# Optimization experiments

Hardware: AMD Instinct MI355X
Metric: run time of the kernel (lower is better)

Reference implementation:

```python
import math
import jax, jax.numpy as jnp
import numpy as np

D, DK, DV = 256, 256, 256

def setup_inputs() -> dict:
    key = jax.random.key(0)
    ks = jax.random.split(key, 7)
    s = 1.0 / math.sqrt(D)
    return {
        "x": jax.random.normal(ks[0], (4, 4096, D), dtype=jnp.float32),
        "Wq": jax.random.uniform(ks[1], (D, DK), jnp.float32, -s, s),
        "bq": jax.random.uniform(ks[2], (DK,), jnp.float32, -s, s),
        "Wk": jax.random.uniform(ks[3], (D, DK), jnp.float32, -s, s),
        "bk": jax.random.uniform(ks[4], (DK,), jnp.float32, -s, s),
        "Wv": jax.random.uniform(ks[5], (D, DV), jnp.float32, -s, s),
        "bv": jax.random.uniform(ks[6], (DV,), jnp.float32, -s, s),
    }

def reference(x, Wq, bq, Wk, bk, Wv, bv):
    # x: [B, S, D]
    q = x @ Wq + bq            # [B, S, DK]
    k = x @ Wk + bk            # [B, S, DK]
    v = x @ Wv + bv            # [B, S, DV]
    scores = jnp.einsum('bqd,bkd->bqk', q, k) / math.sqrt(DK)  # [B, S, S]
    S = x.shape[1]
    causal = jnp.tril(jnp.ones((S, S), dtype=bool))  # True = keep
    scores = jnp.where(causal, scores, -jnp.inf)
    attn = jax.nn.softmax(scores, axis=-1)
    return jnp.einsum('bqk,bkd->bqd', attn, v)  # [B, S, DV]
```

## Files before the change

### kernel.cpp

```cpp
#include <hip/hip_runtime.h>
#include <cmath>

#define LOG2E 1.4426950408889634f

typedef __attribute__((ext_vector_type(8))) __bf16 bf16x8;
typedef __attribute__((ext_vector_type(4))) float f32x4;
typedef __attribute__((ext_vector_type(16))) float f32x16;
typedef __attribute__((ext_vector_type(4))) float float4v;
typedef __attribute__((ext_vector_type(8))) unsigned short ushort8;
typedef __attribute__((ext_vector_type(4))) unsigned int uint4v;
typedef __attribute__((ext_vector_type(2))) int int2v;

__device__ __forceinline__ unsigned short f2bf(float f) {
  unsigned int u = __builtin_bit_cast(unsigned int, f);
  u += 0x7fffu + ((u >> 16) & 1u);
  return (unsigned short)(u >> 16);
}

__device__ __forceinline__ unsigned int cvtpk(float lo, float hi) {
  unsigned int r;
  asm volatile("v_cvt_pk_bf16_f32 %0, %1, %2" : "=v"(r) : "v"(lo), "v"(hi));
  return r;
}

__device__ __forceinline__ void gload_lds16(const unsigned short* g, unsigned short* l) {
  __builtin_amdgcn_global_load_lds(
      (const __attribute__((address_space(1))) unsigned int*)(const void*)g,
      (__attribute__((address_space(3))) unsigned int*)(void*)l, 16, 0, 0);
}

__global__ __launch_bounds__(256) void prep_w_kernel(
    const float* __restrict__ Wq, const float* __restrict__ Wk,
    const float* __restrict__ Wv, unsigned short* __restrict__ Wt) {
  const int w = blockIdx.y, n = blockIdx.x, k = threadIdx.x;
  const float* W = (w == 0) ? Wq : ((w == 1) ? Wk : Wv);
  const float s = (w == 0) ? (LOG2E / 16.0f) : 1.0f;
  Wt[w * 65536 + n * 256 + k] = f2bf(W[k * 256 + n] * s);
}

__global__ __launch_bounds__(256) void proj_kernel(
    const float* __restrict__ x, const unsigned short* __restrict__ Wt,
    const float* __restrict__ bq, const float* __restrict__ bk,
    const float* __restrict__ bv,
    unsigned short* __restrict__ q_o, unsigned short* __restrict__ k_o,
    unsigned short* __restrict__ vt_o) {
  const int mt = blockIdx.x;
  const int tid = threadIdx.x;
  const int wid = tid >> 6, lane = tid & 63, g = (lane >> 4) & 3, c = lane & 15;
  const int row_base = mt * 64 + wid * 16;

  bf16x8 a[8];
  const float* xr = x + (size_t)(row_base + c) * 256;
#pragma unroll
  for (int s = 0; s < 8; ++s) {
    const float4v v0 = *(const float4v*)(xr + s * 32 + g * 8);
    const float4v v1 = *(const float4v*)(xr + s * 32 + g * 8 + 4);
    union { bf16x8 v; unsigned short u[8]; } t;
#pragma unroll
    for (int j = 0; j < 4; ++j) { t.u[j] = f2bf(v0[j]); t.u[4 + j] = f2bf(v1[j]); }
    a[s] = t.v;
  }

  const unsigned short* w0 = Wt;
  const unsigned short* w1 = Wt + 65536;
  const unsigned short* w2 = Wt + 131072;

#pragma unroll
  for (int nf = 0; nf < 16; ++nf) {
    f32x4 aq = (f32x4){0.f, 0.f, 0.f, 0.f};
    f32x4 ak = (f32x4){0.f, 0.f, 0.f, 0.f};
    f32x4 av = (f32x4){0.f, 0.f, 0.f, 0.f};
    const unsigned short* r0 = w0 + (size_t)(nf * 16 + c) * 256;
    const unsigned short* r1 = w1 + (size_t)(nf * 16 + c) * 256;
    const unsigned short* r2 = w2 + (size_t)(nf * 16 + c) * 256;
#pragma unroll
    for (int s = 0; s < 8; ++s) {
      bf16x8 b0 = *(const bf16x8*)(r0 + s * 32 + g * 8);
      bf16x8 b1 = *(const bf16x8*)(r1 + s * 32 + g * 8);
      bf16x8 b2 = *(const bf16x8*)(r2 + s * 32 + g * 8);
      aq = __builtin_amdgcn_mfma_f32_16x16x32_bf16(a[s], b0, aq, 0, 0, 0);
      ak = __builtin_amdgcn_mfma_f32_16x16x32_bf16(a[s], b1, ak, 0, 0, 0);
      av = __builtin_amdgcn_mfma_f32_16x16x32_bf16(a[s], b2, av, 0, 0, 0);
    }
    const float bql = bq[nf * 16 + c] * (LOG2E / 16.0f);
    const float bkl = bk[nf * 16 + c];
    const float bvl = bv[nf * 16 + c];
#pragma unroll
    for (int r = 0; r < 4; ++r) {
      const int row = row_base + g * 4 + r;
      q_o[(size_t)row * 256 + nf * 16 + c] = f2bf(aq[r] + bql);
      k_o[(size_t)row * 256 + nf * 16 + c] = f2bf(ak[r] + bkl);
      const int b_ = row >> 12, s_ = row & 4095;
      vt_o[((size_t)b_ * 256 + nf * 16 + c) * 4096 + s_] = f2bf(av[r] + bvl);
    }
  }
}

__global__ __launch_bounds__(256, 2) void attn_kernel(
    const unsigned short* __restrict__ qg, const unsigned short* __restrict__ kg,
    const unsigned short* __restrict__ vtg, float* __restrict__ out) {
  __shared__ unsigned short Klds[64 * 256];
  __shared__ unsigned short Vlds[256 * 64];
  __shared__ float llds[2][32];

  const int tid = threadIdx.x;
  const int wid = tid >> 6, lane = tid & 63;
  const int hi = lane >> 5, q5 = lane & 31;
  const int wk = wid & 1, dh = wid >> 1;
  const int bid = blockIdx.x;
  const int half = bid >> 8, k6 = (bid >> 2) & 63, b = bid & 3;
  const int qt = half ? k6 : 127 - k6;
  const int T = (qt >> 1) + 1;

  const unsigned short* qb = qg + (size_t)b * 4096 * 256;
  const unsigned short* kb = kg + (size_t)b * 4096 * 256;
  const unsigned short* vb = vtg + (size_t)b * 256 * 4096;
  float* outb = out + (size_t)b * 4096 * 256;

  const int q0 = qt * 32;
  const int qrow = q0 + q5;

  int koff[8], voff[8];
#pragma unroll
  for (int i = 0; i < 8; ++i) {
    const int kr = wid * 16 + i * 2 + (lane >> 5);
    const int c8 = (lane & 31) ^ (kr & 7);
    koff[i] = kr * 256 + c8 * 8;
    const int d = wid * 64 + i * 8 + (lane >> 3);
    const int c8v = (lane & 7) ^ (d & 7);
    voff[i] = d * 4096 + c8v * 8;
  }

  auto stage = [&](int t) {
    const unsigned short* kp = kb + t * (64 * 256);
    const unsigned short* vp = vb + t * 64;
#pragma unroll
    for (int i = 0; i < 8; ++i)
      gload_lds16(kp + koff[i], &Klds[(wid * 8 + i) * 512]);
#pragma unroll
    for (int i = 0; i < 8; ++i)
      gload_lds16(vp + voff[i], &Vlds[(wid * 8 + i) * 512]);
  };

  bf16x8 bqf[16];
  {
    const unsigned short* qr = qb + (size_t)qrow * 256;
#pragma unroll
    for (int s = 0; s < 16; ++s) bqf[s] = *(const bf16x8*)(qr + s * 16 + hi * 8);
  }

  float l = 0.f;
  f32x16 o[4];
#pragma unroll
  for (int d = 0; d < 4; ++d)
#pragma unroll
    for (int r = 0; r < 16; ++r) o[d][r] = 0.f;

  const int krow = wk * 32 + q5;
  const int ksw = (krow & 7) << 3;
  const int kbase = krow * 256;

  int kcolr[16];
#pragma unroll
  for (int r = 0; r < 16; ++r) kcolr[r] = wk * 32 + (r & 3) + 8 * (r >> 2) + 4 * hi;

  stage(0);
  for (int t = 0; t < T; ++t) {
    __syncthreads();

    f32x16 sa, sb;
#pragma unroll
    for (int r = 0; r < 16; ++r) { sa[r] = 0.f; sb[r] = 0.f; }
#pragma unroll
    for (int s = 0; s < 8; ++s) {
      bf16x8 ka0 = *(const bf16x8*)(&Klds[(kbase + s * 16 + hi * 8) ^ ksw]);
      bf16x8 ka1 = *(const bf16x8*)(&Klds[(kbase + (s + 8) * 16 + hi * 8) ^ ksw]);
      sa = __builtin_amdgcn_mfma_f32_32x32x16_bf16(ka0, bqf[s], sa, 0, 0, 0);
      sb = __builtin_amdgcn_mfma_f32_32x32x16_bf16(ka1, bqf[s + 8], sb, 0, 0, 0);
    }
    f32x16 sc = sa + sb;

    if (t == T - 1) {
#pragma unroll
      for (int r = 0; r < 16; ++r)
        if (t * 64 + kcolr[r] > qrow) sc[r] = -1e30f;
    }

    float p[16];
#pragma unroll
    for (int r = 0; r < 16; ++r) p[r] = __builtin_amdgcn_exp2f(sc[r]);
    {
      float s0 = (p[0] + p[1]) + (p[2] + p[3]);
      float s1 = (p[4] + p[5]) + (p[6] + p[7]);
      float s2 = (p[8] + p[9]) + (p[10] + p[11]);
      float s3 = (p[12] + p[13]) + (p[14] + p[15]);
      l += (s0 + s1) + (s2 + s3);
    }

    bf16x8 pfrag[2];
#pragma unroll
    for (int s2 = 0; s2 < 2; ++s2) {
      const int base = s2 * 8;
      unsigned int X = cvtpk(p[base + 0], p[base + 1]);
      unsigned int Y = cvtpk(p[base + 2], p[base + 3]);
      unsigned int Z = cvtpk(p[base + 4], p[base + 5]);
      unsigned int W = cvtpk(p[base + 6], p[base + 7]);
#if __has_builtin(__builtin_amdgcn_permlane32_swap)
      int2v rx = __builtin_amdgcn_permlane32_swap((int)X, (int)Z, false, false);
      int2v ry = __builtin_amdgcn_permlane32_swap((int)Y, (int)W, false, false);
      uint4v u = (uint4v){(unsigned)rx[0], (unsigned)ry[0], (unsigned)rx[1], (unsigned)ry[1]};
#else
      const unsigned int Xp = __shfl_xor((int)X, 32);
      const unsigned int Yp = __shfl_xor((int)Y, 32);
      const unsigned int Zp = __shfl_xor((int)Z, 32);
      const unsigned int Wp = __shfl_xor((int)W, 32);
      uint4v u = (uint4v){hi ? Zp : X, hi ? Wp : Y, hi ? Z : Xp, hi ? W : Yp};
#endif
      pfrag[s2] = __builtin_bit_cast(bf16x8, u);
    }

#pragma unroll
    for (int dblk = 0; dblk < 4; ++dblk) {
      const int drow = (dh * 4 + dblk) * 32 + q5;
      const int vsw = (drow & 7) << 3;
      const int vbase = drow * 64 + wk * 32;
#pragma unroll
      for (int s2 = 0; s2 < 2; ++s2) {
        bf16x8 va = *(const bf16x8*)(&Vlds[(vbase + s2 * 16 + hi * 8) ^ vsw]);
        o[dblk] = __builtin_amdgcn_mfma_f32_32x32x16_bf16(va, pfrag[s2], o[dblk], 0, 0, 0);
      }
    }

    if (t + 1 < T) {
      __syncthreads();
      stage(t + 1);
    }
  }

  l += __shfl_xor(l, 32);
  if (dh == 0 && hi == 0) llds[wk][q5] = l;
  __syncthreads();
  const float L = llds[0][q5] + llds[1][q5];
  const float scale = 1.0f / L;

  float* oz = (float*)Klds;
  if (wk == 1) {
#pragma unroll
    for (int dblk = 0; dblk < 4; ++dblk)
#pragma unroll
      for (int r = 0; r < 16; ++r) {
        const int dg = (dh * 4 + dblk) * 32 + (r & 3) + 8 * (r >> 2) + 4 * hi;
        oz[dg * 32 + q5] = o[dblk][r];
      }
  }
  __syncthreads();
  if (wk == 0) {
#pragma unroll
    for (int dblk = 0; dblk < 4; ++dblk) {
#pragma unroll
      for (int q2 = 0; q2 < 4; ++q2) {
        float4v val;
#pragma unroll
        for (int e = 0; e < 4; ++e) {
          const int r = q2 * 4 + e;
          const int dg = (dh * 4 + dblk) * 32 + e + 8 * q2 + 4 * hi;
          val[e] = (o[dblk][r] + oz[dg * 32 + q5]) * scale;
        }
        *(float4v*)(outb + (size_t)qrow * 256 + (dh * 4 + dblk) * 32 + 8 * q2 + 4 * hi) = val;
      }
    }
  }
}

extern "C" void kernel_launch(void* const* d_in, const int* in_sizes, int n_in,
                              void* d_out, int out_size, void* d_ws, size_t ws_size,
                              hipStream_t stream) {
  (void)in_sizes; (void)n_in; (void)out_size; (void)ws_size;
  const float* x  = (const float*)d_in[0];
  const float* Wq = (const float*)d_in[1];
  const float* bq = (const float*)d_in[2];
  const float* Wk = (const float*)d_in[3];
  const float* bk = (const float*)d_in[4];
  const float* Wv = (const float*)d_in[5];
  const float* bv = (const float*)d_in[6];
  float* out = (float*)d_out;

  unsigned short* qs  = (unsigned short*)d_ws;
  unsigned short* ks  = qs  + (size_t)16384 * 256;
  unsigned short* vts = ks  + (size_t)16384 * 256;
  unsigned short* Wt  = vts + (size_t)16384 * 256;

  prep_w_kernel<<<dim3(256, 3), 256, 0, stream>>>(Wq, Wk, Wv, Wt);
  proj_kernel<<<256, 256, 0, stream>>>(x, Wt, bq, bk, bv, qs, ks, vts);
  attn_kernel<<<512, 256, 0, stream>>>(qs, ks, vts, out);
}
```

Measured before the change: 173.1 us.

## Register-prefetch next K/V tile during compute and split projection grid

The attention kernel stops using direct global-to-LDS loads issued after compute. Instead it loads the next K/V tile into registers at the start of each iteration, overlapping the fetch with the QK and PV MFMAs, then writes the tile to swizzled LDS after a barrier. It also raises wave priority around the MFMA blocks and splits the projection kernel over two column halves to double its block count. The cost is extra VGPRs for staging, which may reduce occupancy, and the projection now reconverts x to bf16 twice.

```diff
diff --git a/kernel.cpp b/kernel.cpp
--- a/kernel.cpp
+++ b/kernel.cpp
@@ -23,12 +23,6 @@
   return r;
 }
 
-__device__ __forceinline__ void gload_lds16(const unsigned short* g, unsigned short* l) {
-  __builtin_amdgcn_global_load_lds(
-      (const __attribute__((address_space(1))) unsigned int*)(const void*)g,
-      (__attribute__((address_space(3))) unsigned int*)(void*)l, 16, 0, 0);
-}
-
 __global__ __launch_bounds__(256) void prep_w_kernel(
     const float* __restrict__ Wq, const float* __restrict__ Wk,
     const float* __restrict__ Wv, unsigned short* __restrict__ Wt) {
@@ -45,6 +39,7 @@
     unsigned short* __restrict__ q_o, unsigned short* __restrict__ k_o,
     unsigned short* __restrict__ vt_o) {
   const int mt = blockIdx.x;
+  const int nfh = blockIdx.y;
   const int tid = threadIdx.x;
   const int wid = tid >> 6, lane = tid & 63, g = (lane >> 4) & 3, c = lane & 15;
   const int row_base = mt * 64 + wid * 16;
@@ -66,7 +61,8 @@
   const unsigned short* w2 = Wt + 131072;
 
 #pragma unroll
-  for (int nf = 0; nf < 16; ++nf) {
+  for (int nfi = 0; nfi < 8; ++nfi) {
+    const int nf = nfh * 8 + nfi;
     f32x4 aq = (f32x4){0.f, 0.f, 0.f, 0.f};
     f32x4 ak = (f32x4){0.f, 0.f, 0.f, 0.f};
     f32x4 av = (f32x4){0.f, 0.f, 0.f, 0.f};
@@ -120,26 +116,28 @@
   const int q0 = qt * 32;
   const int qrow = q0 + q5;
 
-  int koff[8], voff[8];
-#pragma unroll
-  for (int i = 0; i < 8; ++i) {
-    const int kr = wid * 16 + i * 2 + (lane >> 5);
-    const int c8 = (lane & 31) ^ (kr & 7);
-    koff[i] = kr * 256 + c8 * 8;
-    const int d = wid * 64 + i * 8 + (lane >> 3);
-    const int c8v = (lane & 7) ^ (d & 7);
-    voff[i] = d * 4096 + c8v * 8;
-  }
-
-  auto stage = [&](int t) {
-    const unsigned short* kp = kb + t * (64 * 256);
-    const unsigned short* vp = vb + t * 64;
-#pragma unroll
-    for (int i = 0; i < 8; ++i)
-      gload_lds16(kp + koff[i], &Klds[(wid * 8 + i) * 512]);
-#pragma unroll
-    for (int i = 0; i < 8; ++i)
-      gload_lds16(vp + voff[i], &Vlds[(wid * 8 + i) * 512]);
+  uint4v kst[8], vst[8];
+  const int krp = lane >> 5, kc8 = lane & 31;
+  const int vrp = lane >> 3, vc8 = lane & 7;
+
+  auto load_tiles = [&](int t) {
+#pragma unroll
+    for (int i = 0; i < 8; ++i) {
+      const int kr = (wid * 8 + i) * 2 + krp;
+      kst[i] = *(const uint4v*)(kb + (size_t)t * 16384 + kr * 256 + kc8 * 8);
+      const int d = (wid * 8 + i) * 8 + vrp;
+      vst[i] = *(const uint4v*)(vb + (size_t)d * 4096 + t * 64 + vc8 * 8);
+    }
+    __builtin_amdgcn_sched_barrier(0);
+  };
+  auto write_tiles = [&]() {
+#pragma unroll
+    for (int i = 0; i < 8; ++i) {
+      const int kr = (wid * 8 + i) * 2 + krp;
+      *(uint4v*)(&Klds[kr * 256 + (kc8 ^ (kr & 7)) * 8]) = kst[i];
+      const int d = (wid * 8 + i) * 8 + vrp;
+      *(uint4v*)(&Vlds[d * 64 + (vc8 ^ (d & 7)) * 8]) = vst[i];
+    }
   };
 
   bf16x8 bqf[16];
@@ -164,13 +162,18 @@
 #pragma unroll
   for (int r = 0; r < 16; ++r) kcolr[r] = wk * 32 + (r & 3) + 8 * (r >> 2) + 4 * hi;
 
-  stage(0);
+  load_tiles(0);
+  write_tiles();
+  __syncthreads();
+
   for (int t = 0; t < T; ++t) {
-    __syncthreads();
+    const bool pf = (t + 1 < T);
+    if (pf) load_tiles(t + 1);
 
     f32x16 sa, sb;
 #pragma unroll
     for (int r = 0; r < 16; ++r) { sa[r] = 0.f; sb[r] = 0.f; }
+    __builtin_amdgcn_s_setprio(1);
 #pragma unroll
     for (int s = 0; s < 8; ++s) {
       bf16x8 ka0 = *(const bf16x8*)(&Klds[(kbase + s * 16 + hi * 8) ^ ksw]);
@@ -178,6 +181,7 @@
       sa = __builtin_amdgcn_mfma_f32_32x32x16_bf16(ka0, bqf[s], sa, 0, 0, 0);
       sb = __builtin_amdgcn_mfma_f32_32x32x16_bf16(ka1, bqf[s + 8], sb, 0, 0, 0);
     }
+    __builtin_amdgcn_s_setprio(0);
     f32x16 sc = sa + sb;
 
     if (t == T - 1) {
@@ -219,6 +223,7 @@
       pfrag[s2] = __builtin_bit_cast(bf16x8, u);
     }
 
+    __builtin_amdgcn_s_setprio(1);
 #pragma unroll
     for (int dblk = 0; dblk < 4; ++dblk) {
       const int drow = (dh * 4 + dblk) * 32 + q5;
@@ -230,10 +235,12 @@
         o[dblk] = __builtin_amdgcn_mfma_f32_32x32x16_bf16(va, pfrag[s2], o[dblk], 0, 0, 0);
       }
     }
-
-    if (t + 1 < T) {
+    __builtin_amdgcn_s_setprio(0);
+
+    __syncthreads();
+    if (pf) {
+      write_tiles();
       __syncthreads();
-      stage(t + 1);
     }
   }
 
@@ -291,6 +298,6 @@
   unsigned short* Wt  = vts + (size_t)16384 * 256;
 
   prep_w_kernel<<<dim3(256, 3), 256, 0, stream>>>(Wq, Wk, Wv, Wt);
-  proj_kernel<<<256, 256, 0, stream>>>(x, Wt, bq, bk, bv, qs, ks, vts);
+  proj_kernel<<<dim3(256, 2), 256, 0, stream>>>(x, Wt, bq, bk, bv, qs, ks, vts);
   attn_kernel<<<512, 256, 0, stream>>>(qs, ks, vts, out);
 }
```

New measurement: 239.3 us. 38.2% more time.

## Double-buffer 32-key attention tiles, drop cross-wave reduction, split projection grid

Applied to the files above, without the earlier changes.

The attention kernel now streams 32-key K/V tiles into two LDS buffers and issues the next tile's load right after the barrier, so loading overlaps compute and one barrier per iteration goes away. Each wave owns 64 output dims over all keys, which removes the final LDS reduction of partial outputs and row sums across waves. The projection kernel is split over two grid columns of output features to double its block count. Smaller key tiles mean more iterations and more loop overhead per query tile, and the V swizzle layout changes.

```diff
diff --git a/kernel.cpp b/kernel.cpp
--- a/kernel.cpp
+++ b/kernel.cpp
@@ -7,7 +7,6 @@
 typedef __attribute__((ext_vector_type(4))) float f32x4;
 typedef __attribute__((ext_vector_type(16))) float f32x16;
 typedef __attribute__((ext_vector_type(4))) float float4v;
-typedef __attribute__((ext_vector_type(8))) unsigned short ushort8;
 typedef __attribute__((ext_vector_type(4))) unsigned int uint4v;
 typedef __attribute__((ext_vector_type(2))) int int2v;
 
@@ -45,6 +44,7 @@
     unsigned short* __restrict__ q_o, unsigned short* __restrict__ k_o,
     unsigned short* __restrict__ vt_o) {
   const int mt = blockIdx.x;
+  const int nfh = blockIdx.y;
   const int tid = threadIdx.x;
   const int wid = tid >> 6, lane = tid & 63, g = (lane >> 4) & 3, c = lane & 15;
   const int row_base = mt * 64 + wid * 16;
@@ -66,7 +66,8 @@
   const unsigned short* w2 = Wt + 131072;
 
 #pragma unroll
-  for (int nf = 0; nf < 16; ++nf) {
+  for (int nfi = 0; nfi < 8; ++nfi) {
+    const int nf = nfh * 8 + nfi;
     f32x4 aq = (f32x4){0.f, 0.f, 0.f, 0.f};
     f32x4 ak = (f32x4){0.f, 0.f, 0.f, 0.f};
     f32x4 av = (f32x4){0.f, 0.f, 0.f, 0.f};
@@ -99,47 +100,46 @@
 __global__ __launch_bounds__(256, 2) void attn_kernel(
     const unsigned short* __restrict__ qg, const unsigned short* __restrict__ kg,
     const unsigned short* __restrict__ vtg, float* __restrict__ out) {
-  __shared__ unsigned short Klds[64 * 256];
-  __shared__ unsigned short Vlds[256 * 64];
-  __shared__ float llds[2][32];
+  __shared__ unsigned short Klds[2][32 * 256];
+  __shared__ unsigned short Vlds[2][256 * 32];
 
   const int tid = threadIdx.x;
   const int wid = tid >> 6, lane = tid & 63;
   const int hi = lane >> 5, q5 = lane & 31;
-  const int wk = wid & 1, dh = wid >> 1;
+  const int dh = wid;
   const int bid = blockIdx.x;
-  const int half = bid >> 8, k6 = (bid >> 2) & 63, b = bid & 3;
-  const int qt = half ? k6 : 127 - k6;
-  const int T = (qt >> 1) + 1;
+  const int c = bid & 255, half = bid >> 8;
+  const int qt = half ? (c >> 2) : (127 - (c >> 2));
+  const int b = c & 3;
+  const int T = qt + 1;
 
   const unsigned short* qb = qg + (size_t)b * 4096 * 256;
   const unsigned short* kb = kg + (size_t)b * 4096 * 256;
   const unsigned short* vb = vtg + (size_t)b * 256 * 4096;
   float* outb = out + (size_t)b * 4096 * 256;
 
-  const int q0 = qt * 32;
-  const int qrow = q0 + q5;
-
-  int koff[8], voff[8];
-#pragma unroll
-  for (int i = 0; i < 8; ++i) {
-    const int kr = wid * 16 + i * 2 + (lane >> 5);
-    const int c8 = (lane & 31) ^ (kr & 7);
-    koff[i] = kr * 256 + c8 * 8;
-    const int d = wid * 64 + i * 8 + (lane >> 3);
-    const int c8v = (lane & 7) ^ (d & 7);
-    voff[i] = d * 4096 + c8v * 8;
-  }
-
-  auto stage = [&](int t) {
-    const unsigned short* kp = kb + t * (64 * 256);
-    const unsigned short* vp = vb + t * 64;
-#pragma unroll
-    for (int i = 0; i < 8; ++i)
-      gload_lds16(kp + koff[i], &Klds[(wid * 8 + i) * 512]);
-#pragma unroll
-    for (int i = 0; i < 8; ++i)
-      gload_lds16(vp + voff[i], &Vlds[(wid * 8 + i) * 512]);
+  const int qrow = qt * 32 + q5;
+
+  int koff[4], voff[4];
+#pragma unroll
+  for (int i = 0; i < 4; ++i) {
+    const int kr = wid * 8 + i * 2 + (lane >> 5);
+    const int cs = (lane & 31) ^ (kr & 7);
+    koff[i] = kr * 256 + cs * 8;
+    const int d = wid * 64 + i * 16 + (lane >> 2);
+    const int cv = (lane & 3) ^ ((d >> 1) & 3);
+    voff[i] = d * 4096 + cv * 8;
+  }
+
+  auto stage = [&](int bufn, int t) {
+    const unsigned short* kp = kb + (size_t)t * 8192;
+    const unsigned short* vp = vb + t * 32;
+#pragma unroll
+    for (int i = 0; i < 4; ++i)
+      gload_lds16(kp + koff[i], &Klds[bufn][(wid * 4 + i) * 512]);
+#pragma unroll
+    for (int i = 0; i < 4; ++i)
+      gload_lds16(vp + voff[i], &Vlds[bufn][(wid * 4 + i) * 512]);
   };
 
   bf16x8 bqf[16];
@@ -150,31 +150,32 @@
   }
 
   float l = 0.f;
-  f32x16 o[4];
-#pragma unroll
-  for (int d = 0; d < 4; ++d)
+  f32x16 o[2];
+#pragma unroll
+  for (int d = 0; d < 2; ++d)
 #pragma unroll
     for (int r = 0; r < 16; ++r) o[d][r] = 0.f;
 
-  const int krow = wk * 32 + q5;
-  const int ksw = (krow & 7) << 3;
-  const int kbase = krow * 256;
+  const int ksw = (q5 & 7) << 3;
+  const int kbase = q5 * 256;
 
   int kcolr[16];
 #pragma unroll
-  for (int r = 0; r < 16; ++r) kcolr[r] = wk * 32 + (r & 3) + 8 * (r >> 2) + 4 * hi;
-
-  stage(0);
+  for (int r = 0; r < 16; ++r) kcolr[r] = (r & 3) + 8 * (r >> 2) + 4 * hi;
+
+  stage(0, 0);
   for (int t = 0; t < T; ++t) {
+    const int bufn = t & 1;
     __syncthreads();
+    if (t + 1 < T) stage(bufn ^ 1, t + 1);
 
     f32x16 sa, sb;
 #pragma unroll
     for (int r = 0; r < 16; ++r) { sa[r] = 0.f; sb[r] = 0.f; }
 #pragma unroll
     for (int s = 0; s < 8; ++s) {
-      bf16x8 ka0 = *(const bf16x8*)(&Klds[(kbase + s * 16 + hi * 8) ^ ksw]);
-      bf16x8 ka1 = *(const bf16x8*)(&Klds[(kbase + (s + 8) * 16 + hi * 8) ^ ksw]);
+      bf16x8 ka0 = *(const bf16x8*)(&Klds[bufn][(kbase + s * 16 + hi * 8) ^ ksw]);
+      bf16x8 ka1 = *(const bf16x8*)(&Klds[bufn][(kbase + (s + 8) * 16 + hi * 8) ^ ksw]);
       sa = __builtin_amdgcn_mfma_f32_32x32x16_bf16(ka0, bqf[s], sa, 0, 0, 0);
       sb = __builtin_amdgcn_mfma_f32_32x32x16_bf16(ka1, bqf[s + 8], sb, 0, 0, 0);
     }
@@ -183,7 +184,7 @@
     if (t == T - 1) {
 #pragma unroll
       for (int r = 0; r < 16; ++r)
-        if (t * 64 + kcolr[r] > qrow) sc[r] = -1e30f;
+        if (t * 32 + kcolr[r] > qrow) sc[r] = -1e30f;
     }
 
     float p[16];
@@ -220,54 +221,29 @@
     }
 
 #pragma unroll
-    for (int dblk = 0; dblk < 4; ++dblk) {
-      const int drow = (dh * 4 + dblk) * 32 + q5;
-      const int vsw = (drow & 7) << 3;
-      const int vbase = drow * 64 + wk * 32;
+    for (int dblk = 0; dblk < 2; ++dblk) {
+      const int drow = dh * 64 + dblk * 32 + q5;
+      const int vsw = (drow >> 1) & 3;
 #pragma unroll
       for (int s2 = 0; s2 < 2; ++s2) {
-        bf16x8 va = *(const bf16x8*)(&Vlds[(vbase + s2 * 16 + hi * 8) ^ vsw]);
+        const int chunk = s2 * 2 + hi;
+        bf16x8 va = *(const bf16x8*)(&Vlds[bufn][drow * 32 + ((chunk ^ vsw) * 8)]);
         o[dblk] = __builtin_amdgcn_mfma_f32_32x32x16_bf16(va, pfrag[s2], o[dblk], 0, 0, 0);
       }
     }
-
-    if (t + 1 < T) {
-      __syncthreads();
-      stage(t + 1);
-    }
   }
 
   l += __shfl_xor(l, 32);
-  if (dh == 0 && hi == 0) llds[wk][q5] = l;
-  __syncthreads();
-  const float L = llds[0][q5] + llds[1][q5];
-  const float scale = 1.0f / L;
-
-  float* oz = (float*)Klds;
-  if (wk == 1) {
-#pragma unroll
-    for (int dblk = 0; dblk < 4; ++dblk)
-#pragma unroll
-      for (int r = 0; r < 16; ++r) {
-        const int dg = (dh * 4 + dblk) * 32 + (r & 3) + 8 * (r >> 2) + 4 * hi;
-        oz[dg * 32 + q5] = o[dblk][r];
-      }
-  }
-  __syncthreads();
-  if (wk == 0) {
-#pragma unroll
-    for (int dblk = 0; dblk < 4; ++dblk) {
-#pragma unroll
-      for (int q2 = 0; q2 < 4; ++q2) {
-        float4v val;
-#pragma unroll
-        for (int e = 0; e < 4; ++e) {
-          const int r = q2 * 4 + e;
-          const int dg = (dh * 4 + dblk) * 32 + e + 8 * q2 + 4 * hi;
-          val[e] = (o[dblk][r] + oz[dg * 32 + q5]) * scale;
-        }
-        *(float4v*)(outb + (size_t)qrow * 256 + (dh * 4 + dblk) * 32 + 8 * q2 + 4 * hi) = val;
-      }
+  const float scale = 1.0f / l;
+#pragma unroll
+  for (int dblk = 0; dblk < 2; ++dblk) {
+#pragma unroll
+    for (int q2 = 0; q2 < 4; ++q2) {
+      float4v val;
+#pragma unroll
+      for (int e = 0; e < 4; ++e) val[e] = o[dblk][q2 * 4 + e] * scale;
+      const int d0 = dh * 64 + dblk * 32 + 8 * q2 + 4 * hi;
+      *(float4v*)(outb + (size_t)qrow * 256 + d0) = val;
     }
   }
 }
@@ -291,6 +267,6 @@
   unsigned short* Wt  = vts + (size_t)16384 * 256;
 
   prep_w_kernel<<<dim3(256, 3), 256, 0, stream>>>(Wq, Wk, Wv, Wt);
-  proj_kernel<<<256, 256, 0, stream>>>(x, Wt, bq, bk, bv, qs, ks, vts);
+  proj_kernel<<<dim3(256, 2), 256, 0, stream>>>(x, Wt, bq, bk, bv, qs, ks, vts);
   attn_kernel<<<512, 256, 0, stream>>>(qs, ks, vts, out);
 }
```

After: 222.6 us. 28.6% more time.

## Split K/V staging to overlap loads with compute and split projection grid

Applied to the files above, without the earlier changes.

The attention loop now stages K and V tiles separately. The next K tile is issued right after the QK^T MFMAs and the next V tile after the PV MFMAs, with explicit vmcnt waits and raw barriers in place of full __syncthreads, so global-to-LDS loads overlap the other half of the compute. s_setprio is raised around the MFMA sections. The projection kernel is also split across two blocks in y, each covering half of the output columns, to double its parallelism at the cost of converting and loading x twice.

```diff
diff --git a/kernel.cpp b/kernel.cpp
--- a/kernel.cpp
+++ b/kernel.cpp
@@ -7,7 +7,6 @@
 typedef __attribute__((ext_vector_type(4))) float f32x4;
 typedef __attribute__((ext_vector_type(16))) float f32x16;
 typedef __attribute__((ext_vector_type(4))) float float4v;
-typedef __attribute__((ext_vector_type(8))) unsigned short ushort8;
 typedef __attribute__((ext_vector_type(4))) unsigned int uint4v;
 typedef __attribute__((ext_vector_type(2))) int int2v;
 
@@ -45,6 +44,7 @@
     unsigned short* __restrict__ q_o, unsigned short* __restrict__ k_o,
     unsigned short* __restrict__ vt_o) {
   const int mt = blockIdx.x;
+  const int nfh = blockIdx.y;
   const int tid = threadIdx.x;
   const int wid = tid >> 6, lane = tid & 63, g = (lane >> 4) & 3, c = lane & 15;
   const int row_base = mt * 64 + wid * 16;
@@ -66,7 +66,8 @@
   const unsigned short* w2 = Wt + 131072;
 
 #pragma unroll
-  for (int nf = 0; nf < 16; ++nf) {
+  for (int nfi = 0; nfi < 8; ++nfi) {
+    const int nf = nfh * 8 + nfi;
     f32x4 aq = (f32x4){0.f, 0.f, 0.f, 0.f};
     f32x4 ak = (f32x4){0.f, 0.f, 0.f, 0.f};
     f32x4 av = (f32x4){0.f, 0.f, 0.f, 0.f};
@@ -108,8 +109,8 @@
   const int hi = lane >> 5, q5 = lane & 31;
   const int wk = wid & 1, dh = wid >> 1;
   const int bid = blockIdx.x;
-  const int half = bid >> 8, k6 = (bid >> 2) & 63, b = bid & 3;
-  const int qt = half ? k6 : 127 - k6;
+  const int half = bid >> 8, c = bid & 255, b = c & 3;
+  const int qt = half ? (c >> 2) : (127 - (c >> 2));
   const int T = (qt >> 1) + 1;
 
   const unsigned short* qb = qg + (size_t)b * 4096 * 256;
@@ -117,8 +118,7 @@
   const unsigned short* vb = vtg + (size_t)b * 256 * 4096;
   float* outb = out + (size_t)b * 4096 * 256;
 
-  const int q0 = qt * 32;
-  const int qrow = q0 + q5;
+  const int qrow = qt * 32 + q5;
 
   int koff[8], voff[8];
 #pragma unroll
@@ -131,12 +131,14 @@
     voff[i] = d * 4096 + c8v * 8;
   }
 
-  auto stage = [&](int t) {
-    const unsigned short* kp = kb + t * (64 * 256);
-    const unsigned short* vp = vb + t * 64;
+  auto stageK = [&](int t) {
+    const unsigned short* kp = kb + (size_t)t * 16384;
 #pragma unroll
     for (int i = 0; i < 8; ++i)
       gload_lds16(kp + koff[i], &Klds[(wid * 8 + i) * 512]);
+  };
+  auto stageV = [&](int t) {
+    const unsigned short* vp = vb + t * 64;
 #pragma unroll
     for (int i = 0; i < 8; ++i)
       gload_lds16(vp + voff[i], &Vlds[(wid * 8 + i) * 512]);
@@ -164,13 +166,18 @@
 #pragma unroll
   for (int r = 0; r < 16; ++r) kcolr[r] = wk * 32 + (r & 3) + 8 * (r >> 2) + 4 * hi;
 
-  stage(0);
+  stageK(0);
+  stageV(0);
+
   for (int t = 0; t < T; ++t) {
-    __syncthreads();
+    asm volatile("s_waitcnt vmcnt(8)" ::: "memory");
+    __builtin_amdgcn_s_barrier();
+    __builtin_amdgcn_sched_barrier(0);
 
     f32x16 sa, sb;
 #pragma unroll
     for (int r = 0; r < 16; ++r) { sa[r] = 0.f; sb[r] = 0.f; }
+    __builtin_amdgcn_s_setprio(1);
 #pragma unroll
     for (int s = 0; s < 8; ++s) {
       bf16x8 ka0 = *(const bf16x8*)(&Klds[(kbase + s * 16 + hi * 8) ^ ksw]);
@@ -178,7 +185,13 @@
       sa = __builtin_amdgcn_mfma_f32_32x32x16_bf16(ka0, bqf[s], sa, 0, 0, 0);
       sb = __builtin_amdgcn_mfma_f32_32x32x16_bf16(ka1, bqf[s + 8], sb, 0, 0, 0);
     }
+    __builtin_amdgcn_s_setprio(0);
     f32x16 sc = sa + sb;
+
+    asm volatile("s_waitcnt lgkmcnt(0)" ::: "memory");
+    __builtin_amdgcn_s_barrier();
+    __builtin_amdgcn_sched_barrier(0);
+    if (t + 1 < T) stageK(t + 1);
 
     if (t == T - 1) {
 #pragma unroll
@@ -219,6 +232,15 @@
       pfrag[s2] = __builtin_bit_cast(bf16x8, u);
     }
 
+    if (t + 1 < T) {
+      asm volatile("s_waitcnt vmcnt(8)" ::: "memory");
+    } else {
+      asm volatile("s_waitcnt vmcnt(0)" ::: "memory");
+    }
+    __builtin_amdgcn_s_barrier();
+    __builtin_amdgcn_sched_barrier(0);
+
+    __builtin_amdgcn_s_setprio(1);
 #pragma unroll
     for (int dblk = 0; dblk < 4; ++dblk) {
       const int drow = (dh * 4 + dblk) * 32 + q5;
@@ -230,11 +252,12 @@
         o[dblk] = __builtin_amdgcn_mfma_f32_32x32x16_bf16(va, pfrag[s2], o[dblk], 0, 0, 0);
       }
     }
-
-    if (t + 1 < T) {
-      __syncthreads();
-      stage(t + 1);
-    }
+    __builtin_amdgcn_s_setprio(0);
+
+    asm volatile("s_waitcnt lgkmcnt(0)" ::: "memory");
+    __builtin_amdgcn_s_barrier();
+    __builtin_amdgcn_sched_barrier(0);
+    if (t + 1 < T) stageV(t + 1);
   }
 
   l += __shfl_xor(l, 32);
@@ -291,6 +314,6 @@
   unsigned short* Wt  = vts + (size_t)16384 * 256;
 
   prep_w_kernel<<<dim3(256, 3), 256, 0, stream>>>(Wq, Wk, Wv, Wt);
-  proj_kernel<<<256, 256, 0, stream>>>(x, Wt, bq, bk, bv, qs, ks, vts);
+  proj_kernel<<<dim3(256, 2), 256, 0, stream>>>(x, Wt, bq, bk, bv, qs, ks, vts);
   attn_kernel<<<512, 256, 0, stream>>>(qs, ks, vts, out);
 }
```

Measured after the change: 172.2 us. About the same (-0.5%).
